# Kernel tuning notes

Measured on AMD Instinct MI355X. Metric: run time of the kernel, lower is better.

The kernel has to match this reference:

```python
import jax, jax.numpy as jnp
import numpy as np

B, N, D_IN, D_OUT = 32, 256, 512, 2048
RANK, K, H_CTRL = 12, 16, 192
RESIDUAL_SCALE = 1.0


def setup_inputs() -> dict:
    key = jax.random.key(0)
    ks = jax.random.split(key, 12)
    x = jax.random.normal(ks[0], (B, N, D_IN), dtype=jnp.float32)
    shared_weight = 0.02 * jax.random.normal(ks[1], (D_OUT, D_IN), dtype=jnp.float32)
    bias = jnp.zeros((D_OUT,), dtype=jnp.float32)
    # orthogonal init for U_0 [out, in] via QR of a Gaussian
    g = jax.random.normal(ks[2], (D_OUT, D_IN), dtype=jnp.float32)
    U0, _ = jnp.linalg.qr(g, mode='reduced')  # columns orthonormal, out>=in
    left_basis = 0.02 * jax.random.normal(ks[3], (K, D_OUT, RANK), dtype=jnp.float32)
    right_basis = 0.02 * jax.random.normal(ks[4], (K, D_IN, RANK), dtype=jnp.float32)
    ctrl_dim = 3 * D_IN  # cls_mean_var pooling
    W1 = (1.0 / np.sqrt(ctrl_dim)) * jax.random.normal(ks[5], (ctrl_dim, H_CTRL), dtype=jnp.float32)
    b1 = jnp.zeros((H_CTRL,), dtype=jnp.float32)
    Wc = (1.0 / np.sqrt(H_CTRL)) * jax.random.normal(ks[6], (H_CTRL, K), dtype=jnp.float32)
    bc = jnp.zeros((K,), dtype=jnp.float32)
    Wg = (1.0 / np.sqrt(H_CTRL)) * jax.random.normal(ks[7], (H_CTRL, 1), dtype=jnp.float32)
    bg = jnp.zeros((1,), dtype=jnp.float32)
    return {"x": x, "shared_weight": shared_weight, "bias": bias, "U0": U0,
            "left_basis": left_basis, "right_basis": right_basis,
            "W1": W1, "b1": b1, "Wc": Wc, "bc": bc, "Wg": Wg, "bg": bg}


def _controller(z, W1, b1, Wc, bc, Wg, bg):
    # MLP controller: coeff head (linear) + gate head (sigmoid)
    h = jax.nn.gelu(z @ W1 + b1)
    coeff = h @ Wc + bc            # [B, K]
    gate = jax.nn.sigmoid(h @ Wg + bg)  # [B, 1]
    return coeff, gate


def reference(x, shared_weight, bias, U0, left_basis, right_basis, W1, b1, Wc, bc, Wg, bg):
    # conditioning signal: cls + mean + var (unbiased=False)
    cls = x[:, 0]
    mean = x.mean(axis=1)
    var = x.var(axis=1)  # population variance, matches unbiased=False
    z = jnp.concatenate([cls, mean, var], axis=-1)  # [B, 3*D_IN]
    coeff, gate = _controller(z, W1, b1, Wc, bc, Wg, bg)

    # tangent dictionary
    raw = jnp.einsum('kmr,kdr->kmd', left_basis, right_basis)        # [K, M, D]
    ut_raw = jnp.einsum('mi,kmj->kij', U0, raw)                       # U0^T @ raw: [K, D, D]
    sym = 0.5 * (ut_raw + jnp.swapaxes(ut_raw, -2, -1))
    tangent = raw - jnp.einsum('mi,kij->kmj', U0, sym)                # [K, M, D]
    norm = jnp.sqrt(jnp.sum(tangent * tangent, axis=(1, 2), keepdims=True))
    tangent = tangent / jnp.maximum(norm, 1e-6)

    # per-sample candidate + QR retraction (Stiefel)
    delta = jnp.einsum('bk,kmd->bmd', coeff, tangent)                 # [B, M, D]
    candidate = U0[None] + RESIDUAL_SCALE * delta
    q, r = jnp.linalg.qr(candidate, mode='reduced')                   # q: [B, M, D]
    sign = jnp.sign(jnp.diagonal(r, axis1=-2, axis2=-1))              # [B, D]
    sign = jnp.where(sign == 0, jnp.ones_like(sign), sign)
    dynamic_weight = q * sign[..., None, :]
    residual_weight = dynamic_weight - U0[None]                       # [B, M, D]

    out = x @ shared_weight.T + bias                                  # [B, N, M]
    residual_out = jnp.einsum('bnd,bmd->bnm', x, residual_weight)     # [B, N, M]
    return out + gate.reshape(-1, 1, 1) * residual_out
```

## Files before the change

### kernel.cpp

```cpp
#include <hip/hip_runtime.h>
#include <math.h>

#define B_    32
#define N_    256
#define DIN   512
#define DOUT  2048
#define RANK_ 12
#define K_    16
#define HC    192
#define CD    1536
#define P1    192
#define P2    384

typedef short short8 __attribute__((ext_vector_type(8)));
typedef float f32x4 __attribute__((ext_vector_type(4)));

__device__ inline short bf16r(float f) {
  unsigned u = __float_as_uint(f);
  unsigned r = (u + 0x7FFFu + ((u >> 16) & 1u)) >> 16;
  return (short)r;
}
__device__ inline float b16f(short s) {
  unsigned u = ((unsigned)(unsigned short)s) << 16;
  return __uint_as_float(u);
}

__global__ __launch_bounds__(256) void k_pre1(const float* __restrict__ x,
                                              const float* __restrict__ leftb,
                                              const float* __restrict__ rightb,
                                              float* __restrict__ sp, float* __restrict__ s2p,
                                              float* __restrict__ Lcat, float* __restrict__ E) {
  int bx = blockIdx.x, t = threadIdx.x;
  if (bx < 256) {
    int b = bx >> 3, c = bx & 7;
    const float* xb = x + (size_t)b * N_ * DIN;
#pragma unroll
    for (int h2 = 0; h2 < 2; ++h2) {
      int d = t + h2 * 256;
      float s = 0.f, s2 = 0.f;
      for (int n = c * 32; n < c * 32 + 32; ++n) {
        float v = xb[(size_t)n * DIN + d];
        s += v; s2 += v * v;
      }
      sp[(size_t)(b * 8 + c) * DIN + d] = s;
      s2p[(size_t)(b * 8 + c) * DIN + d] = s2;
    }
  } else {
    int idx = (bx - 256) * 256 + t;
    const int totL = DOUT * P1;
    const int totR = DIN * P1;
    if (idx < totL) {
      int m = idx / P1, j = idx - m * P1;
      int k = j / RANK_, r = j - k * RANK_;
      Lcat[idx] = leftb[((size_t)k * DOUT + m) * RANK_ + r];
    } else if (idx < totL + totR) {
      int i2 = idx - totL;
      int d = i2 / P1, j = i2 - d * P1;
      int k = j / RANK_, r = j - k * RANK_;
      E[(size_t)d * P2 + j] = rightb[((size_t)k * DIN + d) * RANK_ + r];
    }
  }
}

__device__ inline void gemm_tn_part(const float* __restrict__ A, const float* __restrict__ B,
                                    float* __restrict__ C, int i0, int j0, int kb0, int klen,
                                    int lda, int ldb, int ldc,
                                    float (*As)[33], float (*Bs)[33], int t) {
  int ii = t & 31, j4 = (t >> 5) * 4;
  float acc[4] = {0.f, 0.f, 0.f, 0.f};
  for (int kb = kb0; kb < kb0 + klen; kb += 32) {
    for (int idx = t; idx < 1024; idx += 256) {
      int kk = idx >> 5, c = idx & 31;
      As[kk][c] = A[(size_t)(kb + kk) * lda + i0 + c];
      Bs[kk][c] = B[(size_t)(kb + kk) * ldb + j0 + c];
    }
    __syncthreads();
#pragma unroll 8
    for (int kk = 0; kk < 32; ++kk) {
      float a = As[kk][ii];
#pragma unroll
      for (int q = 0; q < 4; ++q) acc[q] = fmaf(a, Bs[kk][j4 + q], acc[q]);
    }
    __syncthreads();
  }
#pragma unroll
  for (int q = 0; q < 4; ++q) C[(size_t)(i0 + ii) * ldc + j0 + j4 + q] = acc[q];
}

__global__ __launch_bounds__(256) void k_pre2(const float* __restrict__ x,
                                              const float* __restrict__ sp, const float* __restrict__ s2p,
                                              const float* __restrict__ W1, const float* __restrict__ b1,
                                              const float* __restrict__ U0, const float* __restrict__ LcatF,
                                              float* __restrict__ hgel,
                                              float* __restrict__ Ppart, float* __restrict__ GLLpart) {
  int bx = blockIdx.x, t = threadIdx.x;
  __shared__ float As[32][33], Bs[32][33];
  __shared__ float zsh[CD];
  __shared__ float hp[4][64];
  if (bx < 96) {
    int b = bx / 3, jt = bx % 3;
    int j0 = jt * 64;
    for (int d = t; d < CD; d += 256) {
      float v;
      if (d < DIN) {
        v = x[(size_t)b * N_ * DIN + d];
      } else {
        int dd = d & 511;
        float s = 0.f;
#pragma unroll
        for (int c2 = 0; c2 < 8; ++c2) s += sp[(size_t)(b * 8 + c2) * DIN + dd];
        float mean = s * (1.0f / N_);
        if (d < 2 * DIN) v = mean;
        else {
          float s2 = 0.f;
#pragma unroll
          for (int c2 = 0; c2 < 8; ++c2) s2 += s2p[(size_t)(b * 8 + c2) * DIN + dd];
          v = s2 * (1.0f / N_) - mean * mean;
        }
      }
      zsh[d] = v;
    }
    __syncthreads();
    int j = t & 63, kg = t >> 6;
    float a = 0.f;
    for (int d = kg * 384; d < kg * 384 + 384; ++d)
      a = fmaf(zsh[d], W1[(size_t)d * HC + j0 + j], a);
    hp[kg][j] = a;
    __syncthreads();
    if (kg == 0) {
      float acc = hp[0][j] + hp[1][j] + hp[2][j] + hp[3][j] + b1[j0 + j];
      float x3 = acc * acc * acc;
      float hj = 0.5f * acc * (1.0f + tanhf(0.7978845608028654f * (acc + 0.044715f * x3)));
      hgel[b * HC + j0 + j] = hj;
    }
  } else if (bx < 480) {
    int pb = bx - 96;
    int tile = pb % 96, ks = pb / 96;
    gemm_tn_part(U0, LcatF, Ppart + (size_t)ks * 98304, (tile & 15) * 32, (tile >> 4) * 32,
                 ks * 512, 512, DIN, P1, P1, As, Bs, t);
  } else {
    int gb = bx - 480;
    int tile = gb % 36, ks = gb / 36;
    gemm_tn_part(LcatF, LcatF, GLLpart + (size_t)ks * 36864, (tile % 6) * 32, (tile / 6) * 32,
                 ks * 512, 512, P1, P1, P1, As, Bs, t);
  }
}

__global__ __launch_bounds__(256) void k_pre2b(const float* __restrict__ Ppart,
                                               const float* __restrict__ GLLpart,
                                               float* __restrict__ E, float* __restrict__ GLL) {
  int idx = blockIdx.x * 256 + threadIdx.x;
  if (idx < 98304) {
    float s = Ppart[idx] + Ppart[98304 + idx] + Ppart[2 * 98304 + idx] + Ppart[3 * 98304 + idx];
    int d = idx / P1, j = idx - d * P1;
    E[(size_t)d * P2 + P1 + j] = s;
  } else if (idx < 98304 + 36864) {
    int i2 = idx - 98304;
    GLL[i2] = GLLpart[i2] + GLLpart[36864 + i2] + GLLpart[2 * 36864 + i2] + GLLpart[3 * 36864 + i2];
  }
}

__global__ __launch_bounds__(256) void k_pre3(const float* __restrict__ E,
                                              const float* __restrict__ Wsh, const float* __restrict__ U0,
                                              const float* __restrict__ LcatF,
                                              float* __restrict__ GE, short* __restrict__ Bcat,
                                              short* __restrict__ Eb16, short* __restrict__ Etb16) {
  int bx = blockIdx.x, t = threadIdx.x;
  __shared__ float As[32][33], Bs[32][33];
  if (bx < 144) {
    gemm_tn_part(E, E, GE, (bx % 12) * 32, (bx / 12) * 32, 0, DIN, P2, P2, P2, As, Bs, t);
  } else if (bx < 1360) {
    int idx = (bx - 144) * 256 + t;
    int row = idx / 152, g = idx - row * 152;
    const float* src;
    if (g < 64)       src = Wsh + (size_t)row * DIN + g * 8;
    else if (g < 128) src = U0 + (size_t)row * DIN + (g - 64) * 8;
    else              src = LcatF + (size_t)row * P1 + (g - 128) * 8;
    short8 o;
#pragma unroll
    for (int e = 0; e < 8; ++e) o[e] = bf16r(src[e]);
    *(short8*)(Bcat + (size_t)row * 1216 + g * 8) = o;
  } else {
    int idx = (bx - 1360) * 256 + t;
    int d = idx / P2, q = idx - d * P2;
    short v = bf16r(E[idx]);
    Eb16[idx] = v;
    Etb16[(size_t)q * DIN + d] = v;
  }
}

__global__ __launch_bounds__(512) void k_pre4(const float* __restrict__ GLL, const float* __restrict__ GE,
                                              const float* __restrict__ hgel,
                                              const float* __restrict__ Wc, const float* __restrict__ bc,
                                              const float* __restrict__ Wg, const float* __restrict__ bg,
                                              float* __restrict__ gate, float* __restrict__ cp) {
  __shared__ float nrm[16];
  int t = threadIdx.x;
  int k = t >> 5, lane = t & 31;
  float s1 = 0.f, s2 = 0.f, s3 = 0.f;
  for (int idx = lane; idx < RANK_ * RANK_; idx += 32) {
    int r = idx / RANK_, s = idx - r * RANK_;
    int p = k * RANK_ + r, q = k * RANK_ + s;
    float gll = GLL[p * P1 + q];
    float grr = GE[p * P2 + q];
    float gpp = GE[(P1 + p) * P2 + (P1 + q)];
    float gpr = GE[(P1 + p) * P2 + q];
    float gprt = GE[(P1 + q) * P2 + p];
    s1 += gll * grr;
    s2 += gpp * grr;
    s3 += gpr * gprt;
  }
#pragma unroll
  for (int off = 16; off > 0; off >>= 1) {
    s1 += __shfl_down(s1, off, 32);
    s2 += __shfl_down(s2, off, 32);
    s3 += __shfl_down(s3, off, 32);
  }
  if (lane == 0) nrm[k] = sqrtf(fmaxf(s1 - 0.5f * (s2 + s3), 0.0f));
  int bb = t >> 4, kk = t & 15;
  float c = bc[kk];
  const float* hb = hgel + bb * HC;
  for (int q = 0; q < HC; ++q) c = fmaf(hb[q], Wc[q * K_ + kk], c);
  if (t < B_) {
    float g = bg[0];
    const float* hb2 = hgel + t * HC;
    for (int q = 0; q < HC; ++q) g = fmaf(hb2[q], Wg[q], g);
    gate[t] = 1.0f / (1.0f + expf(-g));
  }
  __syncthreads();
  cp[t] = c / fmaxf(nrm[kk], 1e-6f);
}

__global__ __launch_bounds__(256) void k_pre5(const float* __restrict__ GLL, const float* __restrict__ GE,
                                              const float* __restrict__ E, const float* __restrict__ cp,
                                              short* __restrict__ M0b, short* __restrict__ Ecb) {
  int bx = blockIdx.x, t = threadIdx.x;
  if (bx < 576) {
    int idx = bx * 256 + t;
    if (idx >= P2 * P2) return;
    int p = idx / P2, q = idx - p * P2;
    float v;
    if (p < P1) {
      if (q < P1) v = GLL[p * P1 + q] - 0.75f * GE[(P1 + p) * P2 + (P1 + q)];
      else        v = -0.25f * GE[(P1 + p) * P2 + (q - P1)];
    } else {
      if (q < P1) v = -0.25f * GE[(P1 + q) * P2 + (p - P1)];
      else        v = 0.25f * GE[(p - P1) * P2 + (q - P1)];
    }
    M0b[idx] = bf16r(v);
  } else {
    int idx = (bx - 576) * 256 + t;
    int b = idx / (DIN * 48);
    int rem = idx - b * DIN * 48;
    int d = rem / 48, g = rem - d * 48;
    int q0 = g * 8;
    const float* src = E + (size_t)d * P2 + q0;
    const float* cpb = cp + b * K_;
    short8 o;
#pragma unroll
    for (int e = 0; e < 8; ++e) {
      int q = q0 + e;
      int kidx = (q % P1) / RANK_;
      o[e] = bf16r(src[e] * cpb[kidx]);
    }
    *(short8*)(Ecb + ((size_t)b * DIN + d) * P2 + q0) = o;
  }
}

template<int MSZ, int NSZ, int KD>
__global__ __launch_bounds__(256) void k_mf_nt16(const short* __restrict__ A,
                                                 const short* __restrict__ B,
                                                 short* __restrict__ C) {
  int b = blockIdx.z;
  const short* Ab = A + (size_t)b * MSZ * KD;
  short* Cb = C + (size_t)b * MSZ * NSZ;
  int c0 = blockIdx.x * 64, r0 = blockIdx.y * 64;
  __shared__ short As[64][40], Bs[64][40];
  int t = threadIdx.x;
  int l = t & 63, wid = t >> 6;
  int wr = wid >> 1, wc = wid & 1;
  int fr = l & 15, fq = l >> 4;
  int row = t >> 2, cg = t & 3;
  f32x4 acc[2][2] = {};
  for (int kt = 0; kt < KD / 32; ++kt) {
    *(short8*)&As[row][cg * 8] = *(const short8*)(Ab + (size_t)(r0 + row) * KD + kt * 32 + cg * 8);
    *(short8*)&Bs[row][cg * 8] = *(const short8*)(B + (size_t)(c0 + row) * KD + kt * 32 + cg * 8);
    __syncthreads();
    short8 af[2], bf[2];
#pragma unroll
    for (int m = 0; m < 2; ++m) af[m] = *(const short8*)&As[wr * 32 + m * 16 + fr][fq * 8];
#pragma unroll
    for (int n = 0; n < 2; ++n) bf[n] = *(const short8*)&Bs[wc * 32 + n * 16 + fr][fq * 8];
#pragma unroll
    for (int m = 0; m < 2; ++m)
#pragma unroll
      for (int n = 0; n < 2; ++n)
        acc[m][n] = __builtin_amdgcn_mfma_f32_16x16x32_bf16(af[m], bf[n], acc[m][n], 0, 0, 0);
    __syncthreads();
  }
#pragma unroll
  for (int m = 0; m < 2; ++m)
#pragma unroll
    for (int n = 0; n < 2; ++n)
#pragma unroll
      for (int j = 0; j < 4; ++j)
        Cb[(size_t)(r0 + wr * 32 + m * 16 + fq * 4 + j) * NSZ + c0 + wc * 32 + n * 16 + fr] =
            bf16r(acc[m][n][j]);
}

__global__ __launch_bounds__(256) void k_mf_G(const short* __restrict__ H,
                                              const short* __restrict__ Ec,
                                              float* __restrict__ G) {
  int b = blockIdx.z;
  const short* Ab = H + (size_t)b * DIN * P2;
  const short* Bb = Ec + (size_t)b * DIN * P2;
  float* Gb = G + (size_t)b * DIN * DIN;
  int c0 = blockIdx.x * 64, r0 = blockIdx.y * 64;
  __shared__ short As[64][40], Bs[64][40];
  int t = threadIdx.x;
  int l = t & 63, wid = t >> 6;
  int wr = wid >> 1, wc = wid & 1;
  int fr = l & 15, fq = l >> 4;
  int row = t >> 2, cg = t & 3;
  f32x4 acc[2][2] = {};
  for (int kt = 0; kt < P2 / 32; ++kt) {
    *(short8*)&As[row][cg * 8] = *(const short8*)(Ab + (size_t)(r0 + row) * P2 + kt * 32 + cg * 8);
    *(short8*)&Bs[row][cg * 8] = *(const short8*)(Bb + (size_t)(c0 + row) * P2 + kt * 32 + cg * 8);
    __syncthreads();
    short8 af[2], bf[2];
#pragma unroll
    for (int m = 0; m < 2; ++m) af[m] = *(const short8*)&As[wr * 32 + m * 16 + fr][fq * 8];
#pragma unroll
    for (int n = 0; n < 2; ++n) bf[n] = *(const short8*)&Bs[wc * 32 + n * 16 + fr][fq * 8];
#pragma unroll
    for (int m = 0; m < 2; ++m)
#pragma unroll
      for (int n = 0; n < 2; ++n)
        acc[m][n] = __builtin_amdgcn_mfma_f32_16x16x32_bf16(af[m], bf[n], acc[m][n], 0, 0, 0);
    __syncthreads();
  }
#pragma unroll
  for (int m = 0; m < 2; ++m)
#pragma unroll
    for (int n = 0; n < 2; ++n)
#pragma unroll
      for (int j = 0; j < 4; ++j) {
        int gr = r0 + wr * 32 + m * 16 + fq * 4 + j;
        int gc = c0 + wc * 32 + n * 16 + fr;
        Gb[(size_t)gr * DIN + gc] = acc[m][n][j] + (gr == gc ? 1.0f : 0.0f);
      }
}

__global__ __launch_bounds__(64) void k_chol_dp2(float* __restrict__ G, float* __restrict__ Wd,
                                                 int j0) {
  int b = blockIdx.y;
  int role = blockIdx.x;
  float* Gb = G + (size_t)b * DIN * DIN;
  __shared__ float D[64][65];
  __shared__ float Wls[64][65];
  __shared__ float dinvs[64];
  int t = threadIdx.x;
#pragma unroll 8
  for (int i = 0; i < 64; ++i) D[i][t] = Gb[(size_t)(j0 + i) * DIN + j0 + t];
  __syncthreads();
  {
    float col[64];
#pragma unroll
    for (int i = 0; i < 64; ++i) col[i] = D[i][t];
#pragma unroll
    for (int j = 0; j < 64; ++j) {
      float djj = __shfl(col[j], j);
      float rjj = sqrtf(fmaxf(djj, 1e-30f));
      float rinv = 1.0f / rjj;
      if (t == j) col[j] = rjj;
      else if (t > j) col[j] *= rinv;
      float djt = col[j];
#pragma unroll
      for (int i = j + 1; i < 64; ++i) {
        float rji = __shfl(col[j], i);
        if (i <= t) col[i] = fmaf(-rji, djt, col[i]);
      }
    }
#pragma unroll
    for (int i = 0; i < 64; ++i) D[i][t] = (i <= t) ? col[i] : 0.0f;
    dinvs[t] = 1.0f / col[t];
  }
  __syncthreads();
  if (role == 0) {
#pragma unroll 4
    for (int i = 0; i < 64; ++i) Wls[i][t] = 0.0f;
    Wls[t][t] = dinvs[t];
    for (int i = 62; i >= 0; --i) {
      float s = 0.0f;
      for (int j = i + 1; j < 64; ++j) s = fmaf(D[i][j], Wls[j][t], s);
      if (t > i) Wls[i][t] = -s * dinvs[i];
    }
    float* Wp = Wd + ((size_t)b * 8 + (j0 >> 6)) * 4096;
#pragma unroll 4
    for (int i = 0; i < 64; ++i) Wp[i * 64 + t] = Wls[i][t];
  } else {
    int c = j0 + 64 + (role - 1) * 64 + t;
    float a[64];
#pragma unroll
    for (int i = 0; i < 64; ++i) a[i] = Gb[(size_t)(j0 + i) * DIN + c];
#pragma unroll
    for (int j = 0; j < 64; ++j) {
      float aj = a[j] * dinvs[j];
      a[j] = aj;
#pragma unroll
      for (int i = j + 1; i < 64; ++i) a[i] = fmaf(-D[j][i], aj, a[i]);
    }
#pragma unroll
    for (int i = 0; i < 64; ++i) Gb[(size_t)(j0 + i) * DIN + c] = a[i];
  }
}

__global__ __launch_bounds__(256) void k_chol_tr(float* __restrict__ G, int j0, int nt) {
  int b = blockIdx.y;
  int pi = blockIdx.x;
  int ti = 0, accum = 0;
  while (pi >= accum + (nt - ti)) { accum += nt - ti; ++ti; }
  int tc = ti + (pi - accum);
  float* Gb = G + (size_t)b * DIN * DIN;
  __shared__ float As[64][65], Bs[64][65];
  int t = threadIdx.x;
  int ibase = j0 + 64 + ti * 64, cbase = j0 + 64 + tc * 64;
  for (int idx = t; idx < 4096; idx += 256) {
    int j = idx >> 6, c = idx & 63;
    As[j][c] = Gb[(size_t)(j0 + j) * DIN + ibase + c];
    Bs[j][c] = Gb[(size_t)(j0 + j) * DIN + cbase + c];
  }
  __syncthreads();
  int tx = t & 15, ty = t >> 4;
  float acc[4][4] = {};
#pragma unroll 8
  for (int k = 0; k < 64; ++k) {
    float a[4], bv[4];
#pragma unroll
    for (int u = 0; u < 4; ++u) a[u] = As[k][ty * 4 + u];
#pragma unroll
    for (int v = 0; v < 4; ++v) bv[v] = Bs[k][tx * 4 + v];
#pragma unroll
    for (int u = 0; u < 4; ++u)
#pragma unroll
      for (int v = 0; v < 4; ++v) acc[u][v] = fmaf(a[u], bv[v], acc[u][v]);
  }
#pragma unroll
  for (int u = 0; u < 4; ++u) {
    size_t ro = (size_t)(ibase + ty * 4 + u) * DIN + cbase + tx * 4;
#pragma unroll
    for (int v = 0; v < 4; ++v) Gb[ro + v] -= acc[u][v];
  }
}

__global__ __launch_bounds__(256) void k_trif(const float* __restrict__ x, const float* __restrict__ G,
                                              const float* __restrict__ Wd, short* __restrict__ ybf,
                                              short* __restrict__ ycb) {
  int b = blockIdx.y;
  int n0 = blockIdx.x * 16;
  const float* R = G + (size_t)b * DIN * DIN;
  const float* xb = x + ((size_t)b * N_ + n0) * DIN;
  __shared__ float Yl[16][517];
  __shared__ float Rs[64][65];
  __shared__ float Wds[64][65];
  __shared__ float Ytmp[16][69];
  int t = threadIdx.x;
  for (int idx = t; idx < 16 * DIN; idx += 256)
    Yl[idx >> 9][idx & 511] = xb[(size_t)(idx >> 9) * DIN + (idx & 511)];
  __syncthreads();
  int r = t & 15, cg = t >> 4;
  for (int p = 7; p >= 0; --p) {
    int j0 = p * 64;
    int kN = DIN - j0 - 64;
    float acc[4] = {0.f, 0.f, 0.f, 0.f};
    for (int kb = 0; kb < kN; kb += 64) {
      for (int idx = t; idx < 4096; idx += 256) {
        int kk = idx & 63, c = idx >> 6;
        Rs[kk][c] = R[(size_t)(j0 + c) * DIN + j0 + 64 + kb + kk];
      }
      __syncthreads();
#pragma unroll 8
      for (int kk = 0; kk < 64; ++kk) {
        float a = Yl[r][j0 + 64 + kb + kk];
#pragma unroll
        for (int v = 0; v < 4; ++v) acc[v] = fmaf(a, Rs[kk][cg * 4 + v], acc[v]);
      }
      __syncthreads();
    }
#pragma unroll
    for (int v = 0; v < 4; ++v) Ytmp[r][cg * 4 + v] = Yl[r][j0 + cg * 4 + v] - acc[v];
    const float* Wp = Wd + ((size_t)b * 8 + p) * 4096;
    for (int idx = t; idx < 4096; idx += 256) Wds[idx >> 6][idx & 63] = Wp[idx];
    __syncthreads();
    float o[4] = {0.f, 0.f, 0.f, 0.f};
#pragma unroll 8
    for (int jj = 0; jj < 64; ++jj) {
      float a = Ytmp[r][jj];
#pragma unroll
      for (int v = 0; v < 4; ++v) o[v] = fmaf(a, Wds[cg * 4 + v][jj], o[v]);
    }
    __syncthreads();
#pragma unroll
    for (int v = 0; v < 4; ++v) Yl[r][j0 + cg * 4 + v] = o[v];
    __syncthreads();
  }
  for (int idx = t; idx < 16 * DIN; idx += 256) {
    int rr = idx >> 9, c = idx & 511;
    float yv = Yl[rr][c];
    float xv = xb[(size_t)rr * DIN + c];
    size_t gi = ((size_t)b * N_ + n0 + rr) * DIN + c;
    ybf[gi] = bf16r(yv);
    ycb[gi] = bf16r(yv - xv);
  }
}

__global__ __launch_bounds__(256) void k_yEuv(const short* __restrict__ A,
                                              const short* __restrict__ B,
                                              const float* __restrict__ cp,
                                              const float* __restrict__ gate,
                                              short* __restrict__ C, short* __restrict__ vb) {
  int b = blockIdx.z;
  const short* Ab = A + (size_t)b * N_ * DIN;
  short* Cb = C + (size_t)b * N_ * P2;
  int c0 = blockIdx.x * 64, r0 = blockIdx.y * 64;
  __shared__ short As[64][40], Bs[64][40];
  __shared__ float cps[K_];
  int t = threadIdx.x;
  if (t < K_) cps[t] = cp[b * K_ + t];
  int l = t & 63, wid = t >> 6;
  int wr = wid >> 1, wc = wid & 1;
  int fr = l & 15, fq = l >> 4;
  int row = t >> 2, cg = t & 3;
  f32x4 acc[2][2] = {};
  __syncthreads();
  for (int kt = 0; kt < DIN / 32; ++kt) {
    *(short8*)&As[row][cg * 8] = *(const short8*)(Ab + (size_t)(r0 + row) * DIN + kt * 32 + cg * 8);
    *(short8*)&Bs[row][cg * 8] = *(const short8*)(B + (size_t)(c0 + row) * DIN + kt * 32 + cg * 8);
    __syncthreads();
    short8 af[2], bf[2];
#pragma unroll
    for (int m = 0; m < 2; ++m) af[m] = *(const short8*)&As[wr * 32 + m * 16 + fr][fq * 8];
#pragma unroll
    for (int n = 0; n < 2; ++n) bf[n] = *(const short8*)&Bs[wc * 32 + n * 16 + fr][fq * 8];
#pragma unroll
    for (int m = 0; m < 2; ++m)
#pragma unroll
      for (int n = 0; n < 2; ++n)
        acc[m][n] = __builtin_amdgcn_mfma_f32_16x16x32_bf16(af[m], bf[n], acc[m][n], 0, 0, 0);
    __syncthreads();
  }
  float gt = gate[b];
#pragma unroll
  for (int m = 0; m < 2; ++m)
#pragma unroll
    for (int n = 0; n < 2; ++n)
#pragma unroll
      for (int j = 0; j < 4; ++j) {
        int gr = r0 + wr * 32 + m * 16 + fq * 4 + j;
        int gc = c0 + wc * 32 + n * 16 + fr;
        float v = acc[m][n][j];
        Cb[(size_t)gr * P2 + gc] = bf16r(v);
        if (gc < P1)
          vb[((size_t)b * N_ + gr) * P1 + gc] = bf16r(gt * cps[gc / RANK_] * v);
      }
}

__global__ __launch_bounds__(256) void k_mf_w(const short* __restrict__ yE16,
                                              const short* __restrict__ Eb,
                                              const short* __restrict__ ycb,
                                              const float* __restrict__ cp,
                                              const float* __restrict__ gate,
                                              short* __restrict__ wb) {
  int b = blockIdx.z;
  const short* yEb = yE16 + (size_t)b * N_ * P2;
  int c0 = blockIdx.x * 64, r0 = blockIdx.y * 64;
  __shared__ short As[64][40], Bs[64][40];
  __shared__ float cps[K_];
  int t = threadIdx.x;
  if (t < K_) cps[t] = 0.5f * cp[b * K_ + t];
  int l = t & 63, wid = t >> 6;
  int wr = wid >> 1, wc = wid & 1;
  int fr = l & 15, fq = l >> 4;
  int row = t >> 2, cg = t & 3;
  f32x4 acc[2][2] = {};
  __syncthreads();
  for (int kt = 0; kt < P2 / 32; ++kt) {
    int ksrc0 = (kt * 32 + P1) % P2;
    short8 raw = *(const short8*)(yEb + (size_t)(r0 + row) * P2 + ksrc0 + cg * 8);
    short8 oa;
#pragma unroll
    for (int e = 0; e < 8; ++e) {
      int q = kt * 32 + cg * 8 + e;
      int kidx = (q % P1) / RANK_;
      oa[e] = bf16r(b16f(raw[e]) * cps[kidx]);
    }
    *(short8*)&As[row][cg * 8] = oa;
    *(short8*)&Bs[row][cg * 8] = *(const short8*)(Eb + (size_t)(c0 + row) * P2 + kt * 32 + cg * 8);
    __syncthreads();
    short8 af[2], bf[2];
#pragma unroll
    for (int m = 0; m < 2; ++m) af[m] = *(const short8*)&As[wr * 32 + m * 16 + fr][fq * 8];
#pragma unroll
    for (int n = 0; n < 2; ++n) bf[n] = *(const short8*)&Bs[wc * 32 + n * 16 + fr][fq * 8];
#pragma unroll
    for (int m = 0; m < 2; ++m)
#pragma unroll
      for (int n = 0; n < 2; ++n)
        acc[m][n] = __builtin_amdgcn_mfma_f32_16x16x32_bf16(af[m], bf[n], acc[m][n], 0, 0, 0);
    __syncthreads();
  }
  float gt = gate[b];
#pragma unroll
  for (int m = 0; m < 2; ++m)
#pragma unroll
    for (int n = 0; n < 2; ++n)
#pragma unroll
      for (int j = 0; j < 4; ++j) {
        int gr = r0 + wr * 32 + m * 16 + fq * 4 + j;
        int gc = c0 + wc * 32 + n * 16 + fr;
        size_t gi = ((size_t)b * N_ + gr) * DIN + gc;
        wb[gi] = bf16r(gt * (b16f(ycb[gi]) - acc[m][n][j]));
      }
}

__device__ inline short8 loadA8(const float* __restrict__ x, const short* __restrict__ wb,
                                const short* __restrict__ vb, int grow, int k0) {
  if (k0 < 512) {
    const float* p = x + (size_t)grow * 512 + k0;
    float4 f0 = *(const float4*)p;
    float4 f1 = *(const float4*)(p + 4);
    short8 o;
    o[0] = bf16r(f0.x); o[1] = bf16r(f0.y); o[2] = bf16r(f0.z); o[3] = bf16r(f0.w);
    o[4] = bf16r(f1.x); o[5] = bf16r(f1.y); o[6] = bf16r(f1.z); o[7] = bf16r(f1.w);
    return o;
  } else if (k0 < 1024) {
    return *(const short8*)(wb + (size_t)grow * 512 + k0 - 512);
  } else {
    return *(const short8*)(vb + (size_t)grow * 192 + k0 - 1024);
  }
}

__global__ __launch_bounds__(256) void k_final(
    const float* __restrict__ x, const short* __restrict__ wb, const short* __restrict__ vb,
    const short* __restrict__ Bcat, const float* __restrict__ bias, float* __restrict__ out) {
  __shared__ short As[2][4096];
  __shared__ short Bs[2][4096];
  int t = threadIdx.x;
  int c0 = blockIdx.x * 128;
  int r0 = blockIdx.y * 128;
  int l = t & 63, wid = t >> 6;
  int wr = wid >> 1, wc = wid & 1;
  int fr = l & 15, fq = l >> 4;
  f32x4 acc[4][4] = {};
  short8 ra0, ra1, rb0, rb1;
  const int row0 = t >> 2, c8 = t & 3;
  const int row1 = row0 + 64;
  ra0 = loadA8(x, wb, vb, r0 + row0, c8 * 8);
  ra1 = loadA8(x, wb, vb, r0 + row1, c8 * 8);
  rb0 = *(const short8*)(Bcat + (size_t)(c0 + row0) * 1216 + c8 * 8);
  rb1 = *(const short8*)(Bcat + (size_t)(c0 + row1) * 1216 + c8 * 8);
  *(short8*)&As[0][row0 * 32 + c8 * 8] = ra0;
  *(short8*)&As[0][row1 * 32 + c8 * 8] = ra1;
  *(short8*)&Bs[0][row0 * 32 + c8 * 8] = rb0;
  *(short8*)&Bs[0][row1 * 32 + c8 * 8] = rb1;
  __syncthreads();
  for (int kt = 0; kt < 38; ++kt) {
    int cur = kt & 1;
    if (kt + 1 < 38) {
      int k0 = (kt + 1) * 32;
      ra0 = loadA8(x, wb, vb, r0 + row0, k0 + c8 * 8);
      ra1 = loadA8(x, wb, vb, r0 + row1, k0 + c8 * 8);
      rb0 = *(const short8*)(Bcat + (size_t)(c0 + row0) * 1216 + k0 + c8 * 8);
      rb1 = *(const short8*)(Bcat + (size_t)(c0 + row1) * 1216 + k0 + c8 * 8);
    }
    short8 af[4], bf[4];
#pragma unroll
    for (int m = 0; m < 4; ++m)
      af[m] = *(const short8*)&As[cur][(wr * 64 + m * 16 + fr) * 32 + fq * 8];
#pragma unroll
    for (int n = 0; n < 4; ++n)
      bf[n] = *(const short8*)&Bs[cur][(wc * 64 + n * 16 + fr) * 32 + fq * 8];
#pragma unroll
    for (int m = 0; m < 4; ++m)
#pragma unroll
      for (int n = 0; n < 4; ++n)
        acc[m][n] = __builtin_amdgcn_mfma_f32_16x16x32_bf16(af[m], bf[n], acc[m][n], 0, 0, 0);
    __syncthreads();
    if (kt + 1 < 38) {
      int nxt = cur ^ 1;
      *(short8*)&As[nxt][row0 * 32 + c8 * 8] = ra0;
      *(short8*)&As[nxt][row1 * 32 + c8 * 8] = ra1;
      *(short8*)&Bs[nxt][row0 * 32 + c8 * 8] = rb0;
      *(short8*)&Bs[nxt][row1 * 32 + c8 * 8] = rb1;
    }
    __syncthreads();
  }
#pragma unroll
  for (int n = 0; n < 4; ++n) {
    int col = c0 + wc * 64 + n * 16 + fr;
    float bv = bias[col];
#pragma unroll
    for (int m = 0; m < 4; ++m) {
      int rbase = r0 + wr * 64 + m * 16 + fq * 4;
#pragma unroll
      for (int j = 0; j < 4; ++j)
        out[(size_t)(rbase + j) * DOUT + col] = acc[m][n][j] + bv;
    }
  }
}

extern "C" void kernel_launch(void* const* d_in, const int* in_sizes, int n_in,
                              void* d_out, int out_size, void* d_ws, size_t ws_size,
                              hipStream_t stream) {
  (void)in_sizes; (void)n_in; (void)out_size; (void)ws_size;
  const float* x     = (const float*)d_in[0];
  const float* Wsh   = (const float*)d_in[1];
  const float* bias  = (const float*)d_in[2];
  const float* U0    = (const float*)d_in[3];
  const float* leftb = (const float*)d_in[4];
  const float* rightb= (const float*)d_in[5];
  const float* W1    = (const float*)d_in[6];
  const float* b1    = (const float*)d_in[7];
  const float* Wc    = (const float*)d_in[8];
  const float* bc    = (const float*)d_in[9];
  const float* Wg    = (const float*)d_in[10];
  const float* bg    = (const float*)d_in[11];
  float* out = (float*)d_out;

  float* wsf = (float*)d_ws;
  float* hgel  = wsf + 0;
  float* gate  = wsf + 49664;
  float* cp    = wsf + 49792;
  float* LcatF = wsf + 50304;
  float* E     = wsf + 443520;
  float* GLL   = wsf + 640128;
  float* GE    = wsf + 676992;
  short* M0b16 = (short*)(wsf + 824448);
  short* Eb16  = (short*)(wsf + 898176);
  short* Etb16 = (short*)(wsf + 996480);
  short* wb    = (short*)(wsf + 1094784);
  short* Ecb   = (short*)(wsf + 3191936);
  short* ybf   = (short*)(wsf + 3191936);
  short* vb    = (short*)(wsf + 5289088);
  short* Hb16  = (short*)(wsf + 6337664);
  short* ycb   = (short*)(wsf + 6337664);
  short* Bcat  = (short*)(wsf + 9483392);
  float* sp      = wsf + 10728576;
  float* s2p     = wsf + 10859648;
  float* Ppart   = wsf + 10990720;
  float* GLLpart = wsf + 11383936;
  float* G = out;
  float* Wd = out + 8388608;
  short* yE16 = (short*)(out + 8388608 + 1048576);

  k_pre1<<<256 + 1920, 256, 0, stream>>>(x, leftb, rightb, sp, s2p, LcatF, E);
  k_pre2<<<624, 256, 0, stream>>>(x, sp, s2p, W1, b1, U0, LcatF, hgel, Ppart, GLLpart);
  k_pre2b<<<528, 256, 0, stream>>>(Ppart, GLLpart, E, GLL);
  k_pre3<<<2128, 256, 0, stream>>>(E, Wsh, U0, LcatF, GE, Bcat, Eb16, Etb16);
  k_pre4<<<1, 512, 0, stream>>>(GLL, GE, hgel, Wc, bc, Wg, bg, gate, cp);
  k_pre5<<<3648, 256, 0, stream>>>(GLL, GE, E, cp, M0b16, Ecb);
  k_mf_nt16<DIN, P2, P2><<<dim3(P2 / 64, DIN / 64, B_), 256, 0, stream>>>(Ecb, M0b16, Hb16);
  k_mf_G<<<dim3(DIN / 64, DIN / 64, B_), 256, 0, stream>>>(Hb16, Ecb, G);
  for (int p = 0; p < 8; ++p) {
    int j0 = p * 64;
    int nt = 7 - p;
    k_chol_dp2<<<dim3(nt + 1, B_), 64, 0, stream>>>(G, Wd, j0);
    if (nt > 0)
      k_chol_tr<<<dim3(nt * (nt + 1) / 2, B_), 256, 0, stream>>>(G, j0, nt);
  }
  k_trif<<<dim3(N_ / 16, B_), 256, 0, stream>>>(x, G, Wd, ybf, ycb);
  k_yEuv<<<dim3(P2 / 64, N_ / 64, B_), 256, 0, stream>>>(ybf, Etb16, cp, gate, yE16, vb);
  k_mf_w<<<dim3(DIN / 64, N_ / 64, B_), 256, 0, stream>>>(yE16, Eb16, ycb, cp, gate, wb);
  k_final<<<dim3(DOUT / 128, (B_ * N_) / 128), 256, 0, stream>>>(x, wb, vb, Bcat, bias, out);
}
```

Baseline: 1.467 ms.

## Store Cholesky factor and inverse blocks in bf16, swizzle trif blocks

The Cholesky panel kernel now also writes a bf16 copy of the triangular factor and of the inverted diagonal blocks. The triangular-solve kernel reads these bf16 copies instead of fp32, halving the global bytes it loads. The trif grid is flattened and swizzled so that consecutive workgroups spread across batches, which may improve L2/XCD locality. The cost is extra bf16 stores in the panel kernel and reduced precision in the solve, which could affect accuracy.

New measurement: 1.457 ms (median of 3 runs). About the same (-0.7%).

```diff
diff --git a/kernel.cpp b/kernel.cpp
--- a/kernel.cpp
+++ b/kernel.cpp
@@ -351,11 +351,12 @@
       }
 }
 
-__global__ __launch_bounds__(64) void k_chol_dp2(float* __restrict__ G, float* __restrict__ Wd,
-                                                 int j0) {
+__global__ __launch_bounds__(64) void k_chol_dp2(float* __restrict__ G, short* __restrict__ Rb,
+                                                 short* __restrict__ Wdb, int j0) {
   int b = blockIdx.y;
   int role = blockIdx.x;
   float* Gb = G + (size_t)b * DIN * DIN;
+  short* Rbb = Rb + (size_t)b * DIN * DIN;
   __shared__ float D[64][65];
   __shared__ float Wls[64][65];
   __shared__ float dinvs[64];
@@ -395,9 +396,9 @@
       for (int j = i + 1; j < 64; ++j) s = fmaf(D[i][j], Wls[j][t], s);
       if (t > i) Wls[i][t] = -s * dinvs[i];
     }
-    float* Wp = Wd + ((size_t)b * 8 + (j0 >> 6)) * 4096;
+    short* Wp = Wdb + ((size_t)b * 8 + (j0 >> 6)) * 4096;
 #pragma unroll 4
-    for (int i = 0; i < 64; ++i) Wp[i * 64 + t] = Wls[i][t];
+    for (int i = 0; i < 64; ++i) Wp[i * 64 + t] = bf16r(Wls[i][t]);
   } else {
     int c = j0 + 64 + (role - 1) * 64 + t;
     float a[64];
@@ -411,7 +412,10 @@
       for (int i = j + 1; i < 64; ++i) a[i] = fmaf(-D[j][i], aj, a[i]);
     }
 #pragma unroll
-    for (int i = 0; i < 64; ++i) Gb[(size_t)(j0 + i) * DIN + c] = a[i];
+    for (int i = 0; i < 64; ++i) {
+      Gb[(size_t)(j0 + i) * DIN + c] = a[i];
+      Rbb[(size_t)(j0 + i) * DIN + c] = bf16r(a[i]);
+    }
   }
 }
 
@@ -453,12 +457,14 @@
   }
 }
 
-__global__ __launch_bounds__(256) void k_trif(const float* __restrict__ x, const float* __restrict__ G,
-                                              const float* __restrict__ Wd, short* __restrict__ ybf,
+__global__ __launch_bounds__(256) void k_trif(const float* __restrict__ x, const short* __restrict__ Rb,
+                                              const short* __restrict__ Wdb, short* __restrict__ ybf,
                                               short* __restrict__ ycb) {
-  int b = blockIdx.y;
-  int n0 = blockIdx.x * 16;
-  const float* R = G + (size_t)b * DIN * DIN;
+  int wg = blockIdx.x;
+  int swz = (wg & 7) * 64 + (wg >> 3);
+  int b = swz >> 4;
+  int n0 = (swz & 15) * 16;
+  const short* Rbb = Rb + (size_t)b * DIN * DIN;
   const float* xb = x + ((size_t)b * N_ + n0) * DIN;
   __shared__ float Yl[16][517];
   __shared__ float Rs[64][65];
@@ -476,7 +482,7 @@
     for (int kb = 0; kb < kN; kb += 64) {
       for (int idx = t; idx < 4096; idx += 256) {
         int kk = idx & 63, c = idx >> 6;
-        Rs[kk][c] = R[(size_t)(j0 + c) * DIN + j0 + 64 + kb + kk];
+        Rs[kk][c] = b16f(Rbb[(size_t)(j0 + c) * DIN + j0 + 64 + kb + kk]);
       }
       __syncthreads();
 #pragma unroll 8
@@ -489,8 +495,8 @@
     }
 #pragma unroll
     for (int v = 0; v < 4; ++v) Ytmp[r][cg * 4 + v] = Yl[r][j0 + cg * 4 + v] - acc[v];
-    const float* Wp = Wd + ((size_t)b * 8 + p) * 4096;
-    for (int idx = t; idx < 4096; idx += 256) Wds[idx >> 6][idx & 63] = Wp[idx];
+    const short* Wp = Wdb + ((size_t)b * 8 + p) * 4096;
+    for (int idx = t; idx < 4096; idx += 256) Wds[idx >> 6][idx & 63] = b16f(Wp[idx]);
     __syncthreads();
     float o[4] = {0.f, 0.f, 0.f, 0.f};
 #pragma unroll 8
@@ -750,8 +756,9 @@
   float* Ppart   = wsf + 10990720;
   float* GLLpart = wsf + 11383936;
   float* G = out;
-  float* Wd = out + 8388608;
-  short* yE16 = (short*)(out + 8388608 + 1048576);
+  short* Rb16 = (short*)(out + 8388608);
+  short* yE16 = (short*)(out + 12582912);
+  short* Wdb16 = (short*)(out + 14155776);
 
   k_pre1<<<256 + 1920, 256, 0, stream>>>(x, leftb, rightb, sp, s2p, LcatF, E);
   k_pre2<<<624, 256, 0, stream>>>(x, sp, s2p, W1, b1, U0, LcatF, hgel, Ppart, GLLpart);
@@ -764,11 +771,11 @@
   for (int p = 0; p < 8; ++p) {
     int j0 = p * 64;
     int nt = 7 - p;
-    k_chol_dp2<<<dim3(nt + 1, B_), 64, 0, stream>>>(G, Wd, j0);
+    k_chol_dp2<<<dim3(nt + 1, B_), 64, 0, stream>>>(G, Rb16, Wdb16, j0);
     if (nt > 0)
       k_chol_tr<<<dim3(nt * (nt + 1) / 2, B_), 256, 0, stream>>>(G, j0, nt);
   }
-  k_trif<<<dim3(N_ / 16, B_), 256, 0, stream>>>(x, G, Wd, ybf, ycb);
+  k_trif<<<512, 256, 0, stream>>>(x, Rb16, Wdb16, ybf, ycb);
   k_yEuv<<<dim3(P2 / 64, N_ / 64, B_), 256, 0, stream>>>(ybf, Etb16, cp, gate, yE16, vb);
   k_mf_w<<<dim3(DIN / 64, N_ / 64, B_), 256, 0, stream>>>(yE16, Eb16, ycb, cp, gate, wb);
   k_final<<<dim3(DOUT / 128, (B_ * N_) / 128), 256, 0, stream>>>(x, wb, vb, Bcat, bias, out);
```
